# Kernel tuning notes

Measured on AMD Instinct MI355X. Metric: run time of the kernel, lower is better.

Reference implementation:

```python
import jax, jax.numpy as jnp
import numpy as np

D_MODEL = 1024
NUM_HEADS = 16
HEAD_DIM = D_MODEL // NUM_HEADS
LN_EPS = 1e-3  # Keras LayerNormalization default epsilon


def setup_inputs() -> dict:
    key = jax.random.key(0)
    ks = jax.random.split(key, 7)
    s = 1.0 / np.sqrt(D_MODEL)
    return {
        "x": jax.random.normal(ks[0], (2, 2048, D_MODEL), dtype=jnp.float32),
        "Wq": jax.random.normal(ks[1], (D_MODEL, D_MODEL), dtype=jnp.float32) * s,
        "bq": jnp.zeros((D_MODEL,), dtype=jnp.float32),
        "Wk": jax.random.normal(ks[2], (D_MODEL, D_MODEL), dtype=jnp.float32) * s,
        "bk": jnp.zeros((D_MODEL,), dtype=jnp.float32),
        "Wv": jax.random.normal(ks[3], (D_MODEL, D_MODEL), dtype=jnp.float32) * s,
        "bv": jnp.zeros((D_MODEL,), dtype=jnp.float32),
        "ln_gamma": jnp.ones((D_MODEL,), dtype=jnp.float32),
        "ln_beta": jnp.zeros((D_MODEL,), dtype=jnp.float32),
    }


def _split_heads(t):
    # [B, S, D] -> [B, H, S, Dh]; matches tf.split(axis=2)+concat(axis=0) math
    B, S, D = t.shape
    return t.reshape(B, S, NUM_HEADS, HEAD_DIM).transpose(0, 2, 1, 3)


def reference(x, Wq, bq, Wk, bk, Wv, bv, ln_gamma, ln_beta):
    Q = _split_heads(x @ Wq + bq)   # [B,H,S,Dh]
    K = _split_heads(x @ Wk + bk)
    V = _split_heads(x @ Wv + bv)
    scale = 1.0 / jnp.sqrt(jnp.asarray(HEAD_DIM, dtype=x.dtype))
    scores = jnp.einsum("bhqd,bhkd->bhqk", Q, K) * scale
    probs = jax.nn.softmax(scores, axis=-1)  # dropout is identity at inference
    ctx = jnp.einsum("bhqk,bhkd->bhqd", probs, V)
    out = ctx.transpose(0, 2, 1, 3).reshape(x.shape)  # merge heads -> [B,S,D]
    out = out + x  # residual
    mean = jnp.mean(out, axis=-1, keepdims=True)
    var = jnp.mean(jnp.square(out - mean), axis=-1, keepdims=True)
    return (out - mean) * jax.lax.rsqrt(var + LN_EPS) * ln_gamma + ln_beta
```

## Files before the change

### kernel.cpp

```cpp
#include <hip/hip_runtime.h>
#include <stdint.h>

#define D_MODEL 1024
#define SEQ     2048
#define BATCH   2
#define NHEADS  16
#define HDIM    64
#define ROWS    (BATCH*SEQ)

typedef __attribute__((ext_vector_type(8)))  short short8;
typedef __attribute__((ext_vector_type(4)))  float f32x4;
typedef __attribute__((ext_vector_type(16))) float f32x16;
typedef __attribute__((ext_vector_type(4)))  short short4v;

__device__ __forceinline__ unsigned short f2bf(float f){
  union { float f; unsigned int u; } v; v.f = f;
  unsigned int r = v.u + 0x7fffu + ((v.u >> 16) & 1u);
  return (unsigned short)(r >> 16);
}

__device__ __forceinline__ void gload16(const void* g, void* l){
  __builtin_amdgcn_global_load_lds((__attribute__((address_space(1))) void*)(uintptr_t)g,
                                   (__attribute__((address_space(3))) void*)l, 16, 0, 0);
}

__global__ __launch_bounds__(256) void cvt_x(const float* __restrict__ x,
                                             unsigned short* __restrict__ xb){
  const int i = blockIdx.x*256 + threadIdx.x;
  float4 v = ((const float4*)x)[i];
  short4v o;
  o[0] = (short)f2bf(v.x); o[1] = (short)f2bf(v.y);
  o[2] = (short)f2bf(v.z); o[3] = (short)f2bf(v.w);
  ((short4v*)xb)[i] = o;
}

__global__ __launch_bounds__(256) void wtrans(const float* __restrict__ Wq,
                                              const float* __restrict__ Wk,
                                              const float* __restrict__ Wv,
                                              unsigned short* __restrict__ Wt){
  const float* W = (blockIdx.z==0)?Wq:((blockIdx.z==1)?Wk:Wv);
  unsigned short* dst = Wt + (size_t)blockIdx.z*1048576;
  __shared__ float tile[32][33];
  const int tx = threadIdx.x & 31, ty = threadIdx.x >> 5;
  const int n0 = blockIdx.x*32, k0 = blockIdx.y*32;
  #pragma unroll
  for (int j=0;j<32;j+=8)
    tile[ty+j][tx] = W[(size_t)(k0+ty+j)*D_MODEL + n0+tx];
  __syncthreads();
  #pragma unroll
  for (int j=0;j<32;j+=8)
    dst[(size_t)(n0+ty+j)*D_MODEL + k0+tx] = f2bf(tile[tx][ty+j]);
}

__global__ __launch_bounds__(256) void qkv_gemm(
    const unsigned short* __restrict__ xb, const unsigned short* __restrict__ wtb,
    const float* __restrict__ bq, const float* __restrict__ bk, const float* __restrict__ bv,
    unsigned short* __restrict__ qb, unsigned short* __restrict__ kbuf,
    unsigned short* __restrict__ vbuf)
{
  __shared__ unsigned short As[128*32];
  __shared__ unsigned short Bs[128*32];
  const int mat = blockIdx.z;
  const unsigned short* wt = wtb + (size_t)mat*1048576;
  const float* bias = (mat==0)?bq:((mat==1)?bk:bv);
  unsigned short* outp = (mat==0)?qb:((mat==1)?kbuf:vbuf);
  const float osc = (mat==0)?0.18033688011112042f:1.0f;
  const int bm = blockIdx.x, bn = blockIdx.y;
  const int t = threadIdx.x, w = t>>6, lane = t&63;
  const int g = lane>>4, l15 = lane&15;
  const int wm = w>>1, wn = w&1;

  const int srow = (w<<5) + (lane>>2);
  const int scol = (lane&3)*8;

  f32x4 acc[4][4];
  #pragma unroll
  for (int i=0;i<4;++i)
    #pragma unroll
    for (int j=0;j<4;++j) acc[i][j] = (f32x4){0.f,0.f,0.f,0.f};

  for (int kt=0; kt<32; ++kt){
    const int k0 = kt*32;
    #pragma unroll
    for (int j=0;j<2;++j){
      gload16(xb + (size_t)(bm*128 + srow + j*16)*D_MODEL + k0 + scol, &As[(w<<10)+(j<<9)]);
      gload16(wt + (size_t)(bn*128 + srow + j*16)*D_MODEL + k0 + scol, &Bs[(w<<10)+(j<<9)]);
    }
    __syncthreads();
    short8 a[4], b[4];
    #pragma unroll
    for (int mr=0;mr<4;++mr) a[mr] = *(const short8*)&As[(wm*64 + mr*16 + l15)*32 + g*8];
    #pragma unroll
    for (int nr=0;nr<4;++nr) b[nr] = *(const short8*)&Bs[(wn*64 + nr*16 + l15)*32 + g*8];
    #pragma unroll
    for (int mr=0;mr<4;++mr)
      #pragma unroll
      for (int nr=0;nr<4;++nr)
        acc[mr][nr] = __builtin_amdgcn_mfma_f32_16x16x32_bf16(a[mr], b[nr], acc[mr][nr], 0,0,0);
    __syncthreads();
  }
  #pragma unroll
  for (int mr=0;mr<4;++mr){
    const int rowb = bm*128 + wm*64 + mr*16 + g*4;
    #pragma unroll
    for (int nr=0;nr<4;++nr){
      const int col = bn*128 + wn*64 + nr*16 + l15;
      const float bsv = bias[col];
      const int h = col>>6, d = col&63;
      #pragma unroll
      for (int r=0;r<4;++r){
        const int m = rowb + r;
        const int b_ = m>>11, s = m&2047;
        outp[(((size_t)(b_*NHEADS + h))*SEQ + s)*HDIM + d] = f2bf((acc[mr][nr][r] + bsv)*osc);
      }
    }
  }
}

__global__ __launch_bounds__(256) void vtrans(const unsigned short* __restrict__ vb,
                                              unsigned short* __restrict__ vt){
  __shared__ unsigned short tile[64*72];
  const int bh = blockIdx.y;
  const int s0 = blockIdx.x*64;
  const int t = threadIdx.x;
  {
    const int s_loc = t>>2, d0 = (t&3)*16;
    const unsigned short* src = vb + ((size_t)bh*SEQ + s0 + s_loc)*HDIM + d0;
    *(short8*)&tile[s_loc*72 + d0]     = *(const short8*)src;
    *(short8*)&tile[s_loc*72 + d0 + 8] = *(const short8*)(src+8);
  }
  __syncthreads();
  {
    const int d = t>>2, sc = (t&3)*16;
    short8 o0, o1;
    #pragma unroll
    for (int j=0;j<8;++j){
      o0[j] = (short)tile[(sc+j)*72 + d];
      o1[j] = (short)tile[(sc+8+j)*72 + d];
    }
    unsigned short* dst = vt + ((size_t)bh*HDIM + d)*SEQ + s0 + sc;
    *(short8*)dst     = o0;
    *(short8*)(dst+8) = o1;
  }
}

__global__ __launch_bounds__(256, 2) void attn_fwd(
  const unsigned short* __restrict__ Qb, const unsigned short* __restrict__ Kb,
  const unsigned short* __restrict__ Vtb, float* __restrict__ ctx)
{
  __shared__ unsigned short Ks[2][4096];
  __shared__ unsigned short Vs[2][4096];
  const int lin = blockIdx.x;
  const int bh = (lin&7)*4 + (lin>>7);
  const int q0 = ((lin>>3)&15)*128;
  const int t = threadIdx.x, w = t>>6, lane = t&63;
  const int l31 = lane&31, hi = lane>>5;
  const bool hb = (hi!=0);
  const unsigned short* Qh  = Qb  + (size_t)bh*SEQ*HDIM;
  const unsigned short* Kh  = Kb  + (size_t)bh*SEQ*HDIM;
  const unsigned short* Vth = Vtb + (size_t)bh*HDIM*SEQ;

  const int qrow = q0 + w*32 + l31;
  short8 qf[4];
  #pragma unroll
  for (int dht=0;dht<4;++dht)
    qf[dht] = *(const short8*)&Qh[(size_t)qrow*HDIM + dht*16 + hi*8];

  const int srow0 = t>>3,        srow1 = (256+t)>>3;
  const int skk0  = ((t&7)<<3) ^ ((srow0&7)<<3);
  const int skk1  = ((t&7)<<3) ^ ((srow1&7)<<3);
  const int rx    = l31&7;

  short8 vones;
  #pragma unroll
  for (int j=0;j<8;++j) vones[j] = (short)0x3F80;

  float m = -1e30f;
  f32x16 rs, o0, o1;
  #pragma unroll
  for (int r=0;r<16;++r){ rs[r]=0.f; o0[r]=0.f; o1[r]=0.f; }

#define STAGE(buf, ktile) do {                                                    \
    const int kb_ = (ktile)*64;                                                   \
    gload16(&Kh[(size_t)(kb_ + srow0)*HDIM + skk0], &Ks[buf][(w*64)*8]);          \
    gload16(&Kh[(size_t)(kb_ + srow1)*HDIM + skk1], &Ks[buf][(256 + w*64)*8]);    \
    gload16(&Vth[(size_t)srow0*SEQ + kb_ + skk0],   &Vs[buf][(w*64)*8]);          \
    gload16(&Vth[(size_t)srow1*SEQ + kb_ + skk1],   &Vs[buf][(256 + w*64)*8]);    \
  } while(0)

  STAGE(0, 0);
  __syncthreads();
  int cur = 0;

  for (int kt=0; kt<32; ++kt){
    if (kt < 31) STAGE(cur^1, kt+1);

    f32x16 s0, s1;
    #pragma unroll
    for (int r=0;r<16;++r){ s0[r]=0.f; s1[r]=0.f; }
    __builtin_amdgcn_s_setprio(1);
    #pragma unroll
    for (int dht=0;dht<4;++dht){
      short8 kf = *(const short8*)&Ks[cur][l31*64 + (((dht<<1)|hi) ^ rx)*8];
      s0 = __builtin_amdgcn_mfma_f32_32x32x16_bf16(kf, qf[dht], s0, 0,0,0);
    }
    #pragma unroll
    for (int dht=0;dht<4;++dht){
      short8 kf = *(const short8*)&Ks[cur][(32+l31)*64 + (((dht<<1)|hi) ^ rx)*8];
      s1 = __builtin_amdgcn_mfma_f32_32x32x16_bf16(kf, qf[dht], s1, 0,0,0);
    }
    __builtin_amdgcn_s_setprio(0);

    float rmx = s0[0];
    #pragma unroll
    for (int r=1;r<16;++r) rmx = fmaxf(rmx, s0[r]);
    #pragma unroll
    for (int r=0;r<16;++r) rmx = fmaxf(rmx, s1[r]);
    if (!__all(rmx - m <= 8.0f)){
      float fm = fmaxf(rmx, __shfl_xor(rmx, 32));
      float nm = fmaxf(m, fm);
      float fsc = exp2f(m - nm);
      m = nm;
      #pragma unroll
      for (int r=0;r<16;++r){
        const int cr = (r&3) + ((r>>2)<<3) + (hi<<2);
        const float fr = __shfl(fsc, cr);
        rs[r] *= fr; o0[r] *= fr; o1[r] *= fr;
      }
    }

    unsigned int u[8], v[8];
    #pragma unroll
    for (int i=0;i<8;++i){
      const float a0 = exp2f(s0[2*i]   - m);
      const float a1 = exp2f(s0[2*i+1] - m);
      const float b0 = exp2f(s1[2*i]   - m);
      const float b1 = exp2f(s1[2*i+1] - m);
      asm("v_cvt_pk_bf16_f32 %0, %1, %2" : "=v"(u[i]) : "v"(a0), "v"(a1));
      asm("v_cvt_pk_bf16_f32 %0, %1, %2" : "=v"(v[i]) : "v"(b0), "v"(b1));
    }
    unsigned int su[8], sv[8];
    #pragma unroll
    for (int i=0;i<8;++i){
      su[i] = (unsigned int)__shfl_xor((int)u[i], 32);
      sv[i] = (unsigned int)__shfl_xor((int)v[i], 32);
    }
    union U8 { unsigned int w[4]; short8 s; };
    short8 pa[4];
    {
      U8 a; a.w[0]=hb?su[2]:u[0]; a.w[1]=hb?su[3]:u[1]; a.w[2]=hb?u[2]:su[0]; a.w[3]=hb?u[3]:su[1]; pa[0]=a.s;
      U8 b; b.w[0]=hb?su[6]:u[4]; b.w[1]=hb?su[7]:u[5]; b.w[2]=hb?u[6]:su[4]; b.w[3]=hb?u[7]:su[5]; pa[1]=b.s;
      U8 c; c.w[0]=hb?sv[2]:v[0]; c.w[1]=hb?sv[3]:v[1]; c.w[2]=hb?v[2]:sv[0]; c.w[3]=hb?v[3]:sv[1]; pa[2]=c.s;
      U8 d; d.w[0]=hb?sv[6]:v[4]; d.w[1]=hb?sv[7]:v[5]; d.w[2]=hb?v[6]:sv[4]; d.w[3]=hb?v[7]:sv[5]; pa[3]=d.s;
    }

    __builtin_amdgcn_s_setprio(1);
    #pragma unroll
    for (int kb=0;kb<4;++kb){
      short8 vf0 = *(const short8*)&Vs[cur][l31*64      + (((kb<<1)|hi) ^ rx)*8];
      short8 vf1 = *(const short8*)&Vs[cur][(32+l31)*64 + (((kb<<1)|hi) ^ rx)*8];
      o0 = __builtin_amdgcn_mfma_f32_32x32x16_bf16(pa[kb], vf0, o0, 0,0,0);
      o1 = __builtin_amdgcn_mfma_f32_32x32x16_bf16(pa[kb], vf1, o1, 0,0,0);
      rs = __builtin_amdgcn_mfma_f32_32x32x16_bf16(pa[kb], vones, rs, 0,0,0);
    }
    __builtin_amdgcn_s_setprio(0);

    if (kt < 31){ __syncthreads(); cur ^= 1; }
  }
#undef STAGE

  const int b_ = bh>>4, h = bh&15;
  #pragma unroll
  for (int r=0;r<16;++r){
    const int cr = (r&3) + ((r>>2)<<3) + (hi<<2);
    const int s = q0 + w*32 + cr;
    float* dst = &ctx[((size_t)(b_*SEQ + s))*D_MODEL + h*64];
    const float inv = 1.0f / rs[r];
    dst[l31]      = o0[r] * inv;
    dst[32 + l31] = o1[r] * inv;
  }
}

__global__ __launch_bounds__(256) void resid_ln(
  const float* __restrict__ ctx, const float* __restrict__ x,
  const float* __restrict__ gamma, const float* __restrict__ beta,
  float* __restrict__ out)
{
  const int row = blockIdx.x, t = threadIdx.x;
  const size_t base = (size_t)row*D_MODEL;
  float4 c  = ((const float4*)(ctx + base))[t];
  float4 xr = ((const float4*)(x   + base))[t];
  float4 v; v.x=c.x+xr.x; v.y=c.y+xr.y; v.z=c.z+xr.z; v.w=c.w+xr.w;
  float s  = v.x+v.y+v.z+v.w;
  float ss = v.x*v.x+v.y*v.y+v.z*v.z+v.w*v.w;
  #pragma unroll
  for (int m=1;m<64;m<<=1){ s += __shfl_xor(s,m); ss += __shfl_xor(ss,m); }
  __shared__ float red[8];
  const int w = t>>6;
  if ((t&63)==0){ red[w] = s; red[4+w] = ss; }
  __syncthreads();
  s  = red[0]+red[1]+red[2]+red[3];
  ss = red[4]+red[5]+red[6]+red[7];
  const float mean = s*(1.f/D_MODEL);
  const float var  = ss*(1.f/D_MODEL) - mean*mean;
  const float rstd = rsqrtf(var + 1e-3f);
  float4 gv = ((const float4*)gamma)[t], bv = ((const float4*)beta)[t];
  float4 ov;
  ov.x=(v.x-mean)*rstd*gv.x+bv.x; ov.y=(v.y-mean)*rstd*gv.y+bv.y;
  ov.z=(v.z-mean)*rstd*gv.z+bv.z; ov.w=(v.w-mean)*rstd*gv.w+bv.w;
  ((float4*)(out + base))[t] = ov;
}

extern "C" void kernel_launch(void* const* d_in, const int* in_sizes, int n_in,
                              void* d_out, int out_size, void* d_ws, size_t ws_size,
                              hipStream_t stream){
  const float* x     = (const float*)d_in[0];
  const float* Wq    = (const float*)d_in[1];
  const float* bq    = (const float*)d_in[2];
  const float* Wk    = (const float*)d_in[3];
  const float* bk    = (const float*)d_in[4];
  const float* Wv    = (const float*)d_in[5];
  const float* bv    = (const float*)d_in[6];
  const float* gamma = (const float*)d_in[7];
  const float* beta  = (const float*)d_in[8];
  float* out = (float*)d_out;

  char* ws = (char*)d_ws;
  unsigned short* xb  = (unsigned short*)(ws);
  unsigned short* wtb = (unsigned short*)(ws + 8388608);
  unsigned short* qb  = (unsigned short*)(ws + 14680064);
  unsigned short* kb  = (unsigned short*)(ws + 23068672);
  unsigned short* vb  = (unsigned short*)(ws + 31457280);
  float* ctx          = (float*)(ws + 39845888);
  unsigned short* vtb = (unsigned short*)(ws);

  hipLaunchKernelGGL(cvt_x,    dim3(ROWS*D_MODEL/1024), dim3(256), 0, stream, x, xb);
  hipLaunchKernelGGL(wtrans,   dim3(32,32,3),           dim3(256), 0, stream, Wq, Wk, Wv, wtb);
  hipLaunchKernelGGL(qkv_gemm, dim3(32,8,3),            dim3(256), 0, stream,
                     xb, wtb, bq, bk, bv, qb, kb, vb);
  hipLaunchKernelGGL(vtrans,   dim3(SEQ/64, BATCH*NHEADS), dim3(256), 0, stream, vb, vtb);
  hipLaunchKernelGGL(attn_fwd, dim3(512),               dim3(256), 0, stream, qb, kb, vtb, ctx);
  hipLaunchKernelGGL(resid_ln, dim3(ROWS),              dim3(256), 0, stream, ctx, x, gamma, beta, out);
}
```

Before: 131.5 us.

## Streamline attention inner loop: permlane swaps, raw exp, max tree, unroll by two

Rewrites the attention inner loop. P fragments are now exchanged between half-waves with v_permlane32_swap instead of shuffles and selects. exp2f is replaced by raw v_exp_f32, the row max becomes a three-input max tree, and the loop is unrolled by two so the LDS buffer index is a compile-time constant. These cut VALU and cross-lane work in the softmax section, at the cost of larger code and possibly more register pressure.

```diff
diff --git a/kernel.cpp b/kernel.cpp
--- a/kernel.cpp
+++ b/kernel.cpp
@@ -17,6 +17,16 @@
   union { float f; unsigned int u; } v; v.f = f;
   unsigned int r = v.u + 0x7fffu + ((v.u >> 16) & 1u);
   return (unsigned short)(r >> 16);
+}
+
+__device__ __forceinline__ float fast_exp2(float x){
+  float r;
+  asm("v_exp_f32 %0, %1" : "=v"(r) : "v"(x));
+  return r;
+}
+
+__device__ __forceinline__ float f3(float a, float b, float c){
+  return fmaxf(fmaxf(a,b),c);
 }
 
 __device__ __forceinline__ void gload16(const void* g, void* l){
@@ -155,7 +165,6 @@
   const int q0 = ((lin>>3)&15)*128;
   const int t = threadIdx.x, w = t>>6, lane = t&63;
   const int l31 = lane&31, hi = lane>>5;
-  const bool hb = (hi!=0);
   const unsigned short* Qh  = Qb  + (size_t)bh*SEQ*HDIM;
   const unsigned short* Kh  = Kb  + (size_t)bh*SEQ*HDIM;
   const unsigned short* Vth = Vtb + (size_t)bh*HDIM*SEQ;
@@ -188,85 +197,91 @@
     gload16(&Vth[(size_t)srow1*SEQ + kb_ + skk1],   &Vs[buf][(256 + w*64)*8]);    \
   } while(0)
 
+#define BODY(CUR, KT) do {                                                        \
+    if ((KT) < 31) STAGE((CUR)^1, (KT)+1);                                        \
+                                       \
+    f32x16 s0, s1;                                                                \
+    _Pragma("unroll")                                                             \
+    for (int r=0;r<16;++r){ s0[r]=0.f; s1[r]=0.f; }                               \
+    __builtin_amdgcn_s_setprio(1);                                                \
+    _Pragma("unroll")                                                             \
+    for (int dht=0;dht<4;++dht){                                                  \
+      short8 kf = *(const short8*)&Ks[CUR][l31*64 + (((dht<<1)|hi) ^ rx)*8];      \
+      s0 = __builtin_amdgcn_mfma_f32_32x32x16_bf16(kf, qf[dht], s0, 0,0,0);       \
+    }                                                                             \
+    _Pragma("unroll")                                                             \
+    for (int dht=0;dht<4;++dht){                                                  \
+      short8 kf = *(const short8*)&Ks[CUR][(32+l31)*64 + (((dht<<1)|hi) ^ rx)*8]; \
+      s1 = __builtin_amdgcn_mfma_f32_32x32x16_bf16(kf, qf[dht], s1, 0,0,0);       \
+    }                                                                             \
+    __builtin_amdgcn_s_setprio(0);                                                \
+                        \
+    float a0=f3(s0[0],s0[1],s0[2]),  a1=f3(s0[3],s0[4],s0[5]);                    \
+    float a2=f3(s0[6],s0[7],s0[8]),  a3=f3(s0[9],s0[10],s0[11]);                  \
+    float a4=f3(s0[12],s0[13],s0[14]), a5=f3(s0[15],s1[0],s1[1]);                 \
+    float a6=f3(s1[2],s1[3],s1[4]),  a7=f3(s1[5],s1[6],s1[7]);                    \
+    float a8=f3(s1[8],s1[9],s1[10]), a9=f3(s1[11],s1[12],s1[13]);                 \
+    float a10=fmaxf(s1[14],s1[15]);                                               \
+    float rmx = f3(f3(a0,a1,a2), f3(a3,a4,a5), f3(f3(a6,a7,a8), a9, a10));        \
+    if (!__all(rmx - m <= 8.0f)){                                                 \
+      float fm = fmaxf(rmx, __shfl_xor(rmx, 32));                                 \
+      float nm = fmaxf(m, fm);                                                    \
+      float fsc = fast_exp2(m - nm);                                              \
+      m = nm;                                                                     \
+      _Pragma("unroll")                                                           \
+      for (int r=0;r<16;++r){                                                     \
+        const int cr = (r&3) + ((r>>2)<<3) + (hi<<2);                             \
+        const float fr = __shfl(fsc, cr);                                         \
+        rs[r] *= fr; o0[r] *= fr; o1[r] *= fr;                                    \
+      }                                                                           \
+    }                                                                             \
+                \
+    unsigned int u[8], vv[8];                                                     \
+    _Pragma("unroll")                                                             \
+    for (int i=0;i<8;++i){                                                        \
+      float e0 = fast_exp2(s0[2*i]   - m);                                        \
+      float e1 = fast_exp2(s0[2*i+1] - m);                                        \
+      float e2 = fast_exp2(s1[2*i]   - m);                                        \
+      float e3 = fast_exp2(s1[2*i+1] - m);                                        \
+      asm("v_cvt_pk_bf16_f32 %0, %1, %2" : "=v"(u[i])  : "v"(e0), "v"(e1));       \
+      asm("v_cvt_pk_bf16_f32 %0, %1, %2" : "=v"(vv[i]) : "v"(e2), "v"(e3));       \
+    }                                                                             \
+    asm("v_permlane32_swap_b32 %0, %1" : "+v"(u[0]),  "+v"(u[2]));                \
+    asm("v_permlane32_swap_b32 %0, %1" : "+v"(u[1]),  "+v"(u[3]));                \
+    asm("v_permlane32_swap_b32 %0, %1" : "+v"(u[4]),  "+v"(u[6]));                \
+    asm("v_permlane32_swap_b32 %0, %1" : "+v"(u[5]),  "+v"(u[7]));                \
+    asm("v_permlane32_swap_b32 %0, %1" : "+v"(vv[0]), "+v"(vv[2]));               \
+    asm("v_permlane32_swap_b32 %0, %1" : "+v"(vv[1]), "+v"(vv[3]));               \
+    asm("v_permlane32_swap_b32 %0, %1" : "+v"(vv[4]), "+v"(vv[6]));               \
+    asm("v_permlane32_swap_b32 %0, %1" : "+v"(vv[5]), "+v"(vv[7]));               \
+    union U8 { unsigned int wq[4]; short8 s; };                                   \
+    short8 pa[4];                                                                 \
+    { U8 x; x.wq[0]=u[0];  x.wq[1]=u[1];  x.wq[2]=u[2];  x.wq[3]=u[3];  pa[0]=x.s; } \
+    { U8 x; x.wq[0]=u[4];  x.wq[1]=u[5];  x.wq[2]=u[6];  x.wq[3]=u[7];  pa[1]=x.s; } \
+    { U8 x; x.wq[0]=vv[0]; x.wq[1]=vv[1]; x.wq[2]=vv[2]; x.wq[3]=vv[3]; pa[2]=x.s; } \
+    { U8 x; x.wq[0]=vv[4]; x.wq[1]=vv[5]; x.wq[2]=vv[6]; x.wq[3]=vv[7]; pa[3]=x.s; } \
+                                          \
+    __builtin_amdgcn_s_setprio(1);                                                \
+    _Pragma("unroll")                                                             \
+    for (int kb=0;kb<4;++kb){                                                     \
+      short8 vf0 = *(const short8*)&Vs[CUR][l31*64      + (((kb<<1)|hi) ^ rx)*8]; \
+      short8 vf1 = *(const short8*)&Vs[CUR][(32+l31)*64 + (((kb<<1)|hi) ^ rx)*8]; \
+      o0 = __builtin_amdgcn_mfma_f32_32x32x16_bf16(pa[kb], vf0, o0, 0,0,0);       \
+      o1 = __builtin_amdgcn_mfma_f32_32x32x16_bf16(pa[kb], vf1, o1, 0,0,0);       \
+      rs = __builtin_amdgcn_mfma_f32_32x32x16_bf16(pa[kb], vones, rs, 0,0,0);     \
+    }                                                                             \
+    __builtin_amdgcn_s_setprio(0);                                                \
+    if ((KT) < 31) __syncthreads();                                               \
+  } while(0)
+
   STAGE(0, 0);
   __syncthreads();
-  int cur = 0;
-
-  for (int kt=0; kt<32; ++kt){
-    if (kt < 31) STAGE(cur^1, kt+1);
-
-    f32x16 s0, s1;
-    #pragma unroll
-    for (int r=0;r<16;++r){ s0[r]=0.f; s1[r]=0.f; }
-    __builtin_amdgcn_s_setprio(1);
-    #pragma unroll
-    for (int dht=0;dht<4;++dht){
-      short8 kf = *(const short8*)&Ks[cur][l31*64 + (((dht<<1)|hi) ^ rx)*8];
-      s0 = __builtin_amdgcn_mfma_f32_32x32x16_bf16(kf, qf[dht], s0, 0,0,0);
-    }
-    #pragma unroll
-    for (int dht=0;dht<4;++dht){
-      short8 kf = *(const short8*)&Ks[cur][(32+l31)*64 + (((dht<<1)|hi) ^ rx)*8];
-      s1 = __builtin_amdgcn_mfma_f32_32x32x16_bf16(kf, qf[dht], s1, 0,0,0);
-    }
-    __builtin_amdgcn_s_setprio(0);
-
-    float rmx = s0[0];
-    #pragma unroll
-    for (int r=1;r<16;++r) rmx = fmaxf(rmx, s0[r]);
-    #pragma unroll
-    for (int r=0;r<16;++r) rmx = fmaxf(rmx, s1[r]);
-    if (!__all(rmx - m <= 8.0f)){
-      float fm = fmaxf(rmx, __shfl_xor(rmx, 32));
-      float nm = fmaxf(m, fm);
-      float fsc = exp2f(m - nm);
-      m = nm;
-      #pragma unroll
-      for (int r=0;r<16;++r){
-        const int cr = (r&3) + ((r>>2)<<3) + (hi<<2);
-        const float fr = __shfl(fsc, cr);
-        rs[r] *= fr; o0[r] *= fr; o1[r] *= fr;
-      }
-    }
-
-    unsigned int u[8], v[8];
-    #pragma unroll
-    for (int i=0;i<8;++i){
-      const float a0 = exp2f(s0[2*i]   - m);
-      const float a1 = exp2f(s0[2*i+1] - m);
-      const float b0 = exp2f(s1[2*i]   - m);
-      const float b1 = exp2f(s1[2*i+1] - m);
-      asm("v_cvt_pk_bf16_f32 %0, %1, %2" : "=v"(u[i]) : "v"(a0), "v"(a1));
-      asm("v_cvt_pk_bf16_f32 %0, %1, %2" : "=v"(v[i]) : "v"(b0), "v"(b1));
-    }
-    unsigned int su[8], sv[8];
-    #pragma unroll
-    for (int i=0;i<8;++i){
-      su[i] = (unsigned int)__shfl_xor((int)u[i], 32);
-      sv[i] = (unsigned int)__shfl_xor((int)v[i], 32);
-    }
-    union U8 { unsigned int w[4]; short8 s; };
-    short8 pa[4];
-    {
-      U8 a; a.w[0]=hb?su[2]:u[0]; a.w[1]=hb?su[3]:u[1]; a.w[2]=hb?u[2]:su[0]; a.w[3]=hb?u[3]:su[1]; pa[0]=a.s;
-      U8 b; b.w[0]=hb?su[6]:u[4]; b.w[1]=hb?su[7]:u[5]; b.w[2]=hb?u[6]:su[4]; b.w[3]=hb?u[7]:su[5]; pa[1]=b.s;
-      U8 c; c.w[0]=hb?sv[2]:v[0]; c.w[1]=hb?sv[3]:v[1]; c.w[2]=hb?v[2]:sv[0]; c.w[3]=hb?v[3]:sv[1]; pa[2]=c.s;
-      U8 d; d.w[0]=hb?sv[6]:v[4]; d.w[1]=hb?sv[7]:v[5]; d.w[2]=hb?v[6]:sv[4]; d.w[3]=hb?v[7]:sv[5]; pa[3]=d.s;
-    }
-
-    __builtin_amdgcn_s_setprio(1);
-    #pragma unroll
-    for (int kb=0;kb<4;++kb){
-      short8 vf0 = *(const short8*)&Vs[cur][l31*64      + (((kb<<1)|hi) ^ rx)*8];
-      short8 vf1 = *(const short8*)&Vs[cur][(32+l31)*64 + (((kb<<1)|hi) ^ rx)*8];
-      o0 = __builtin_amdgcn_mfma_f32_32x32x16_bf16(pa[kb], vf0, o0, 0,0,0);
-      o1 = __builtin_amdgcn_mfma_f32_32x32x16_bf16(pa[kb], vf1, o1, 0,0,0);
-      rs = __builtin_amdgcn_mfma_f32_32x32x16_bf16(pa[kb], vones, rs, 0,0,0);
-    }
-    __builtin_amdgcn_s_setprio(0);
-
-    if (kt < 31){ __syncthreads(); cur ^= 1; }
-  }
+
+  for (int kt2=0; kt2<32; kt2+=2){
+    BODY(0, kt2);
+    BODY(1, kt2+1);
+  }
+#undef BODY
 #undef STAGE
 
   const int b_ = bh>>4, h = bh&15;
```

Result: faster. 113.7 us (-13.5%).
